# Performance work log

Hardware: AMD Instinct MI355X
Metric: run time of the kernel (lower is better)

Reference implementation:

```python
import jax, jax.numpy as jnp
import numpy as np

B, F = 4096, 128          # batch, num fields
L = 3                     # att_layer_num
H1, H2 = 256, 128         # dnn_hidden_units


def setup_inputs() -> dict:
    key = jax.random.key(0)
    ks = jax.random.split(key, 10)
    X = jax.random.normal(ks[0], (B, F), dtype=jnp.float32)
    # InteractingLayer params: embedding_size=1, head_num=1 -> (1,1) matrices, std=0.05
    wq = jax.random.normal(ks[1], (L, 1, 1), dtype=jnp.float32) * 0.05
    wk = jax.random.normal(ks[2], (L, 1, 1), dtype=jnp.float32) * 0.05
    wv = jax.random.normal(ks[3], (L, 1, 1), dtype=jnp.float32) * 0.05
    wr = jax.random.normal(ks[4], (L, 1, 1), dtype=jnp.float32) * 0.05
    # DNN: Linear(F->H1), Linear(H1->H2) with init_std=1e-4 weights, zero-ish bias
    W1 = jax.random.normal(ks[5], (F, H1), dtype=jnp.float32) * 1e-4
    b1 = jnp.zeros((H1,), dtype=jnp.float32)
    W2 = jax.random.normal(ks[6], (H1, H2), dtype=jnp.float32) * 1e-4
    b2 = jnp.zeros((H2,), dtype=jnp.float32)
    # dnn_linear: Linear(H2 -> 1, bias=False)
    Wf = jax.random.normal(ks[7], (H2, 1), dtype=jnp.float32) * 0.05
    return {"X": X, "wq": wq, "wk": wk, "wv": wv, "wr": wr,
            "W1": W1, "b1": b1, "W2": W2, "b2": b2, "Wf": Wf}


def _interact(x, wq, wk, wv, wr):
    # x: (B, F, 1); w*: (1, 1). head_num=1, att_embedding_size=1, no scaling.
    q = jnp.einsum('bfe,ed->bfd', x, wq)
    k = jnp.einsum('bfe,ed->bfd', x, wk)
    v = jnp.einsum('bfe,ed->bfd', x, wv)
    scores = jax.nn.softmax(jnp.einsum('bfd,bgd->bfg', q, k), axis=-1)  # (B,F,F)
    out = jnp.einsum('bfg,bgd->bfd', scores, v)
    out = out + jnp.einsum('bfe,ed->bfd', x, wr)  # use_res residual
    return jax.nn.relu(out)


def reference(X, wq, wk, wv, wr, W1, b1, W2, b2, Wf):
    att = X[..., None]  # (B, F, 1)
    for i in range(L):
        att = _interact(att, wq[i], wk[i], wv[i], wr[i])
    h = att.reshape(att.shape[0], -1)          # (B, F)
    h = jax.nn.relu(h @ W1 + b1)               # (B, H1)
    h = jax.nn.relu(h @ W2 + b2)               # (B, H2)
    return h @ Wf                              # (B, 1)
```

## Files before the change

### kernel.cpp

```cpp
#include <hip/hip_runtime.h>
#include <hip/hip_bf16.h>


#define FDIM 128
#define NLAYER 3
#define RPB 8
#define H1 256
#define H2 128

__global__ __launch_bounds__(1024) void autoint_fused(
    const float* __restrict__ X,
    const float* __restrict__ wq, const float* __restrict__ wk,
    const float* __restrict__ wv, const float* __restrict__ wr,
    const float* __restrict__ W1, const float* __restrict__ b1,
    const float* __restrict__ W2, const float* __restrict__ b2,
    const float* __restrict__ Wf,
    float* __restrict__ out)
{
    __shared__ float sx[RPB][FDIM];
    __shared__ float sh1[RPB][H1];
    __shared__ float part[8192];
    __shared__ float red[RPB][2];

    const int tid = threadIdx.x;
    const int b0  = blockIdx.x * RPB;

    const int r = tid >> 7;
    const int f = tid & 127;
    float xf = X[(b0 + r) * FDIM + f];
    sx[r][f] = xf;
    __syncthreads();

    #pragma unroll
    for (int l = 0; l < NLAYER; ++l) {
        const float c  = wq[l] * wk[l] * 1.4426950408889634f;
        const float vv = wv[l];
        const float rr = wr[l];

        const float a = c * xf;
        float den = 0.f, num = 0.f;

        #pragma unroll 4
        for (int g = 0; g < FDIM; g += 4) {
            float4 xg = *reinterpret_cast<const float4*>(&sx[r][g]);
            float e0 = __builtin_amdgcn_exp2f(a * xg.x);
            float e1 = __builtin_amdgcn_exp2f(a * xg.y);
            float e2 = __builtin_amdgcn_exp2f(a * xg.z);
            float e3 = __builtin_amdgcn_exp2f(a * xg.w);
            den += (e0 + e1) + (e2 + e3);
            num = fmaf(e0, xg.x, num);
            num = fmaf(e1, xg.y, num);
            num = fmaf(e2, xg.z, num);
            num = fmaf(e3, xg.w, num);
        }

        float o = fmaxf(fmaf(rr, xf, vv * num / den), 0.f);
        __syncthreads();
        sx[r][f] = o;
        xf = o;
        __syncthreads();
    }

    {
        const int j  = tid & 255;
        const int kq = tid >> 8;
        float acc[RPB];
        #pragma unroll
        for (int q = 0; q < RPB; ++q) acc[q] = 0.f;

        const int i0 = kq * 32;
        #pragma unroll 8
        for (int ii = 0; ii < 32; ++ii) {
            const int i = i0 + ii;
            const float w = W1[i * H1 + j];
            #pragma unroll
            for (int q = 0; q < RPB; ++q)
                acc[q] = fmaf(sx[q][i], w, acc[q]);
        }
        #pragma unroll
        for (int q = 0; q < RPB; ++q)
            part[kq * 2048 + q * 256 + j] = acc[q];
    }
    __syncthreads();
    {
        #pragma unroll
        for (int idx = tid; idx < RPB * H1; idx += 1024) {
            const int q = idx >> 8, j = idx & 255;
            float s = b1[j] + ((part[idx] + part[2048 + idx]) +
                               (part[4096 + idx] + part[6144 + idx]));
            sh1[q][j] = fmaxf(s, 0.f);
        }
    }
    __syncthreads();

    {
        const int k  = tid & 127;
        const int kq = tid >> 7;
        float acc[RPB];
        #pragma unroll
        for (int q = 0; q < RPB; ++q) acc[q] = 0.f;

        const int j0 = kq * 32;
        #pragma unroll 8
        for (int jj = 0; jj < 32; ++jj) {
            const int j = j0 + jj;
            const float w = W2[j * H2 + k];
            #pragma unroll
            for (int q = 0; q < RPB; ++q)
                acc[q] = fmaf(sh1[q][j], w, acc[q]);
        }
        #pragma unroll
        for (int q = 0; q < RPB; ++q)
            part[kq * 1024 + q * 128 + k] = acc[q];
    }
    __syncthreads();
    {
        const int r2 = tid >> 7;
        const int k  = tid & 127;
        float s = b2[k];
        #pragma unroll
        for (int q = 0; q < 8; ++q)
            s += part[q * 1024 + r2 * 128 + k];
        float p = fmaxf(s, 0.f) * Wf[k];

        #pragma unroll
        for (int off = 32; off >= 1; off >>= 1)
            p += __shfl_down(p, off, 64);
        if ((tid & 63) == 0)
            red[r2][(tid >> 6) & 1] = p;
    }
    __syncthreads();

    if (tid < RPB)
        out[b0 + tid] = red[tid][0] + red[tid][1];
}

extern "C" void kernel_launch(void* const* d_in, const int* in_sizes, int n_in,
                              void* d_out, int out_size, void* d_ws, size_t ws_size,
                              hipStream_t stream) {
    const float* X  = (const float*)d_in[0];
    const float* wq = (const float*)d_in[1];
    const float* wk = (const float*)d_in[2];
    const float* wv = (const float*)d_in[3];
    const float* wr = (const float*)d_in[4];
    const float* W1 = (const float*)d_in[5];
    const float* b1 = (const float*)d_in[6];
    const float* W2 = (const float*)d_in[7];
    const float* b2 = (const float*)d_in[8];
    const float* Wf = (const float*)d_in[9];
    float* out = (float*)d_out;

    const int B = in_sizes[0] / FDIM;
    autoint_fused<<<dim3(B / RPB), dim3(1024), 0, stream>>>(
        X, wq, wk, wv, wr, W1, b1, W2, b2, Wf, out);
}
```

Measured before the change: 128.4 us.

## Halve rows per block, double-buffer attention state, split accumulators

Each block now handles 4 rows with 512 threads, so there are twice as many blocks. Shared memory shrinks and the launch bound is set to 8 blocks per CU to raise occupancy. The attention state is double-buffered in shared memory, which removes one barrier per layer. The softmax sums use two accumulators each to shorten the dependency chains. The MLP weight loads are now reused across only 4 rows instead of 8, so total W1/W2 traffic from cache doubles.

```diff
diff --git a/kernel.cpp b/kernel.cpp
--- a/kernel.cpp
+++ b/kernel.cpp
@@ -4,11 +4,12 @@
 
 #define FDIM 128
 #define NLAYER 3
-#define RPB 8
+#define RPB 4
+#define THREADS 512
 #define H1 256
 #define H2 128
 
-__global__ __launch_bounds__(1024) void autoint_fused(
+__global__ __launch_bounds__(THREADS, 8) void autoint_fused(
     const float* __restrict__ X,
     const float* __restrict__ wq, const float* __restrict__ wk,
     const float* __restrict__ wv, const float* __restrict__ wr,
@@ -17,9 +18,9 @@
     const float* __restrict__ Wf,
     float* __restrict__ out)
 {
-    __shared__ float sx[RPB][FDIM];
+    __shared__ float sx[2][RPB][FDIM];
     __shared__ float sh1[RPB][H1];
-    __shared__ float part[8192];
+    __shared__ float part[2048];
     __shared__ float red[RPB][2];
 
     const int tid = threadIdx.x;
@@ -28,35 +29,36 @@
     const int r = tid >> 7;
     const int f = tid & 127;
     float xf = X[(b0 + r) * FDIM + f];
-    sx[r][f] = xf;
+    sx[0][r][f] = xf;
     __syncthreads();
 
     #pragma unroll
     for (int l = 0; l < NLAYER; ++l) {
+        const int cur = l & 1;
         const float c  = wq[l] * wk[l] * 1.4426950408889634f;
         const float vv = wv[l];
         const float rr = wr[l];
 
         const float a = c * xf;
-        float den = 0.f, num = 0.f;
+        float den0 = 0.f, den1 = 0.f, num0 = 0.f, num1 = 0.f;
 
         #pragma unroll 4
         for (int g = 0; g < FDIM; g += 4) {
-            float4 xg = *reinterpret_cast<const float4*>(&sx[r][g]);
+            float4 xg = *reinterpret_cast<const float4*>(&sx[cur][r][g]);
             float e0 = __builtin_amdgcn_exp2f(a * xg.x);
             float e1 = __builtin_amdgcn_exp2f(a * xg.y);
             float e2 = __builtin_amdgcn_exp2f(a * xg.z);
             float e3 = __builtin_amdgcn_exp2f(a * xg.w);
-            den += (e0 + e1) + (e2 + e3);
-            num = fmaf(e0, xg.x, num);
-            num = fmaf(e1, xg.y, num);
-            num = fmaf(e2, xg.z, num);
-            num = fmaf(e3, xg.w, num);
+            den0 += e0 + e1;
+            den1 += e2 + e3;
+            num0 = fmaf(e0, xg.x, num0);
+            num1 = fmaf(e1, xg.y, num1);
+            num0 = fmaf(e2, xg.z, num0);
+            num1 = fmaf(e3, xg.w, num1);
         }
 
-        float o = fmaxf(fmaf(rr, xf, vv * num / den), 0.f);
-        __syncthreads();
-        sx[r][f] = o;
+        float o = fmaxf(fmaf(rr, xf, vv * (num0 + num1) / (den0 + den1)), 0.f);
+        sx[cur ^ 1][r][f] = o;
         xf = o;
         __syncthreads();
     }
@@ -68,26 +70,25 @@
         #pragma unroll
         for (int q = 0; q < RPB; ++q) acc[q] = 0.f;
 
-        const int i0 = kq * 32;
+        const int i0 = kq * 64;
         #pragma unroll 8
-        for (int ii = 0; ii < 32; ++ii) {
+        for (int ii = 0; ii < 64; ++ii) {
             const int i = i0 + ii;
             const float w = W1[i * H1 + j];
             #pragma unroll
             for (int q = 0; q < RPB; ++q)
-                acc[q] = fmaf(sx[q][i], w, acc[q]);
+                acc[q] = fmaf(sx[1][q][i], w, acc[q]);
         }
         #pragma unroll
         for (int q = 0; q < RPB; ++q)
-            part[kq * 2048 + q * 256 + j] = acc[q];
+            part[kq * 1024 + q * 256 + j] = acc[q];
     }
     __syncthreads();
     {
         #pragma unroll
-        for (int idx = tid; idx < RPB * H1; idx += 1024) {
+        for (int idx = tid; idx < RPB * H1; idx += THREADS) {
             const int q = idx >> 8, j = idx & 255;
-            float s = b1[j] + ((part[idx] + part[2048 + idx]) +
-                               (part[4096 + idx] + part[6144 + idx]));
+            float s = b1[j] + part[idx] + part[1024 + idx];
             sh1[q][j] = fmaxf(s, 0.f);
         }
     }
@@ -95,14 +96,14 @@
 
     {
         const int k  = tid & 127;
-        const int kq = tid >> 7;
+        const int kc = tid >> 7;
         float acc[RPB];
         #pragma unroll
         for (int q = 0; q < RPB; ++q) acc[q] = 0.f;
 
-        const int j0 = kq * 32;
+        const int j0 = kc * 64;
         #pragma unroll 8
-        for (int jj = 0; jj < 32; ++jj) {
+        for (int jj = 0; jj < 64; ++jj) {
             const int j = j0 + jj;
             const float w = W2[j * H2 + k];
             #pragma unroll
@@ -111,23 +112,23 @@
         }
         #pragma unroll
         for (int q = 0; q < RPB; ++q)
-            part[kq * 1024 + q * 128 + k] = acc[q];
+            part[kc * 512 + q * 128 + k] = acc[q];
     }
     __syncthreads();
     {
-        const int r2 = tid >> 7;
+        const int rq = tid >> 7;
         const int k  = tid & 127;
         float s = b2[k];
         #pragma unroll
-        for (int q = 0; q < 8; ++q)
-            s += part[q * 1024 + r2 * 128 + k];
+        for (int kc = 0; kc < 4; ++kc)
+            s += part[kc * 512 + rq * 128 + k];
         float p = fmaxf(s, 0.f) * Wf[k];
 
         #pragma unroll
         for (int off = 32; off >= 1; off >>= 1)
             p += __shfl_down(p, off, 64);
         if ((tid & 63) == 0)
-            red[r2][(tid >> 6) & 1] = p;
+            red[rq][(tid >> 6) & 1] = p;
     }
     __syncthreads();
 
@@ -151,6 +152,6 @@
     float* out = (float*)d_out;
 
     const int B = in_sizes[0] / FDIM;
-    autoint_fused<<<dim3(B / RPB), dim3(1024), 0, stream>>>(
+    autoint_fused<<<dim3(B / RPB), dim3(THREADS), 0, stream>>>(
         X, wq, wk, wv, wr, W1, b1, W2, b2, Wf, out);
 }
```

Result: faster. 120.1 us (-6.5%).
